# Kernel optimization log

Measured on AMD Instinct MI355X. Metric: run time of the kernel, lower is better.

The kernel has to match this reference:

```python
import jax, jax.numpy as jnp
import numpy as np

N_WIRES = 12
DIM = 2 ** N_WIRES  # 4096 = seq_len * embed_dim

_H = np.array([[1, 1], [1, -1]], dtype=np.complex64) / np.sqrt(2.0)
_CNOT = np.array([[1, 0, 0, 0],
                  [0, 1, 0, 0],
                  [0, 0, 0, 1],
                  [0, 0, 1, 0]], dtype=np.complex64)
_SWAP = np.array([[1, 0, 0, 0],
                  [0, 0, 1, 0],
                  [0, 1, 0, 0],
                  [0, 0, 0, 1]], dtype=np.complex64)

def _cp_mat(theta):
    m = np.eye(4, dtype=np.complex64)
    m[3, 3] = np.exp(1j * theta)
    return m

def _apply_gate(state, U, wires):
    # state: (B,) + (2,)*N_WIRES ; U: (2^k, 2^k) acting on `wires` (wire 0 = MSB = axis 1)
    k = len(wires)
    src = [w + 1 for w in wires]
    dst = list(range(1, k + 1))
    st = jnp.moveaxis(state, src, dst)
    sh = st.shape
    st = st.reshape(sh[0], 2 ** k, -1)
    st = jnp.einsum('ij,bjr->bir', jnp.asarray(U), st)
    return jnp.moveaxis(st.reshape(sh), dst, src)

def _cnot_ring(state):
    for i in range(N_WIRES):
        state = _apply_gate(state, _CNOT, [i, (i + 1) % N_WIRES])
    return state

def _qft(state):
    for m in range(N_WIRES - 1, 0, -1):
        state = _apply_gate(state, _H, [m])
        for i in range(m):
            state = _apply_gate(state, _cp_mat(np.pi / 2 ** (m - i)), [i, m])
    for i in range(N_WIRES // 2):
        state = _apply_gate(state, _SWAP, [i, N_WIRES - i - 1])
    return state

def _full_unitary(state, U):
    # dense 2^n x 2^n unitary over the whole register: psi' = U @ psi
    b = state.shape[0]
    flat = state.reshape(b, DIM)
    return jnp.einsum('ij,bj->bi', U, flat).reshape(state.shape)

def setup_inputs() -> dict:
    key = jax.random.key(0)
    k1, k2, k3 = jax.random.split(key, 3)
    x = jax.random.normal(k1, (128, 64, 64), dtype=jnp.float32)
    scale = DIM ** -0.5  # keep applied matrices roughly norm-preserving
    U_re = jax.random.normal(k2, (4, DIM, DIM), dtype=jnp.float32) * scale
    U_im = jax.random.normal(k3, (4, DIM, DIM), dtype=jnp.float32) * scale
    return {"x": x, "U_re": U_re, "U_im": U_im}

def reference(x, U_re, U_im):
    B, S, E = x.shape
    flat = x.reshape(B, S * E)
    pad = DIM - flat.shape[1]
    if pad > 0:
        flat = jnp.pad(flat, ((0, 0), (0, pad)))
    # StateEncoder: L2-normalize and lift to complex statevector
    norm = jnp.sqrt(jnp.sum(flat * flat, axis=-1, keepdims=True))
    psi = (flat / norm).astype(jnp.complex64)
    state = psi.reshape((B,) + (2,) * N_WIRES)
    U = (U_re + 1j * U_im).astype(jnp.complex64)
    # vqc(0)
    state = _full_unitary(state, U[0])
    state = _cnot_ring(state)
    state = _full_unitary(state, U[1])
    # qft
    state = _qft(state)
    # vqc(1)
    state = _full_unitary(state, U[2])
    state = _cnot_ring(state)
    state = _full_unitary(state, U[3])
    out = jnp.abs(state.reshape(B, DIM))
    return out.reshape(B, S, E)
```

## Files before the change

kernel.cpp:

```cpp
#include <hip/hip_runtime.h>
#include <hip/hip_bf16.h>
#include <math.h>

#define N_WIRES 12
#define DIM     4096
#define BATCH   128
#define BD      (BATCH*DIM)
#define BM      128
#define BN      32
#define BK      64
#define KS      4
#define KCHUNK  (DIM / KS)

typedef __attribute__((ext_vector_type(4))) float f32x4;
typedef __attribute__((ext_vector_type(4))) unsigned int u32x4;
typedef __bf16 bf16x8 __attribute__((ext_vector_type(8)));
typedef __attribute__((ext_vector_type(8))) unsigned short us8;

__device__ __forceinline__ f32x4 mfma16(bf16x8 a, bf16x8 b, f32x4 c){
  return __builtin_amdgcn_mfma_f32_16x16x32_bf16(a, b, c, 0, 0, 0);
}

__device__ __forceinline__ void gload16(const void* g, void* l){
  __builtin_amdgcn_global_load_lds(
    (const __attribute__((address_space(1))) unsigned int*)g,
    (__attribute__((address_space(3))) unsigned int*)l, 16, 0, 0);
}

__device__ __forceinline__ float bf2f(unsigned short u){
  union { unsigned int i; float f; } cv; cv.i = ((unsigned int)u) << 16; return cv.f;
}

__device__ __forceinline__ int swz(int j, int b){
  return (j & ~63) | (((((j >> 3) & 7) ^ (b & 7))) << 3) | (j & 7);
}

__global__ void k_normalize(const float* __restrict__ x, __hip_bfloat16* __restrict__ dst){
  const int b = blockIdx.x, t = threadIdx.x;
  const float4* xr = reinterpret_cast<const float4*>(x + (size_t)b * DIM);
  float4 v[4];
  float ss = 0.f;
  #pragma unroll
  for (int r = 0; r < 4; ++r){
    v[r] = xr[t*4 + r];
    ss += v[r].x*v[r].x + v[r].y*v[r].y + v[r].z*v[r].z + v[r].w*v[r].w;
  }
  #pragma unroll
  for (int off = 32; off > 0; off >>= 1) ss += __shfl_down(ss, off);
  __shared__ float sred[4];
  if ((t & 63) == 0) sred[t >> 6] = ss;
  __syncthreads();
  const float inv = 1.f / sqrtf(sred[0] + sred[1] + sred[2] + sred[3]);
  #pragma unroll
  for (int h = 0; h < 2; ++h){
    union { __bf16 e[8]; us8 s; } pk;
    const float* vv = reinterpret_cast<const float*>(&v[h*2]);
    #pragma unroll
    for (int j = 0; j < 8; ++j) pk.e[j] = (__bf16)(vv[j] * inv);
    const int j0 = t*16 + h*8;
    *reinterpret_cast<us8*>(dst + (size_t)b*DIM + swz(j0, b)) = pk.s;
  }
}

template<bool CIN>
__global__ __launch_bounds__(256, 2) void k_gemm(
    const float* __restrict__ Ure, const float* __restrict__ Uim,
    const __hip_bfloat16* __restrict__ X, __hip_bfloat16* __restrict__ P)
{
  constexpr int NCC = CIN ? 2 : 1;
  constexpr int NT  = KCHUNK / BK;
  __shared__ __bf16 Xs[2][NCC*BM*BK];
  __shared__ __bf16 Us[2][2*BN*BK];
  const int t = threadIdx.x;
  const int lane = t & 63, wid = t >> 6;
  const int n0 = blockIdx.x * BN;
  const int kb = blockIdx.y * KCHUNK;

  const f32x4 z4 = {0.f,0.f,0.f,0.f};
  f32x4 acc[2][2][2];
  #pragma unroll
  for (int mi = 0; mi < 2; ++mi)
    #pragma unroll
    for (int ni = 0; ni < 2; ++ni){ acc[mi][ni][0] = z4; acc[mi][ni][1] = z4; }

  auto stageX = [&](int kk, int bf){
    #pragma unroll
    for (int r = 0; r < NCC*4; ++r){
      const int idx = r*256 + t;
      const int c = idx >> 10, ci = idx & 1023;
      const int row = ci >> 3, sc = ci & 7;
      gload16(X + (size_t)c*BD + (size_t)row*DIM + kb + kk + sc*8, &Xs[bf][idx*8]);
    }
  };
  auto loadU = [&](int kk, float4 (&uv)[4]){
    #pragma unroll
    for (int r = 0; r < 4; ++r){
      const int idx = r*256 + t;
      const int c = idx >> 9, ci = idx & 511;
      const int row = ci >> 4, q = ci & 15;
      const float* us = c ? Uim : Ure;
      uv[r] = *reinterpret_cast<const float4*>(us + (size_t)(n0 + row)*DIM + kb + kk + q*4);
    }
  };
  auto writeU = [&](const float4 (&uv)[4], int bf){
    #pragma unroll
    for (int r = 0; r < 4; ++r){
      const int idx = r*256 + t;
      const int c = idx >> 9, ci = idx & 511;
      const int row = ci >> 4, q = ci & 15;
      union { __bf16 h[4]; unsigned long long u; } pk;
      pk.h[0]=(__bf16)uv[r].x; pk.h[1]=(__bf16)uv[r].y;
      pk.h[2]=(__bf16)uv[r].z; pk.h[3]=(__bf16)uv[r].w;
      const int e = (((q >> 1) ^ (row & 7)) << 3) | ((q & 1) << 2);
      *reinterpret_cast<unsigned long long*>(&Us[bf][c*BN*BK + row*BK + e]) = pk.u;
    }
  };
  auto compute = [&](int bf){
    #pragma unroll
    for (int ks = 0; ks < 2; ++ks){
      const int lc = ks*4 + (lane >> 4);
      bf16x8 ar[2], ai[2], br[2], bi[2];
      #pragma unroll
      for (int mi = 0; mi < 2; ++mi){
        const int row = wid*32 + mi*16 + (lane & 15);
        const int off = row*BK + ((lc ^ (row & 7)) << 3);
        ar[mi] = *reinterpret_cast<const bf16x8*>(&Xs[bf][off]);
        if (CIN) ai[mi] = *reinterpret_cast<const bf16x8*>(&Xs[bf][BM*BK + off]);
      }
      #pragma unroll
      for (int ni = 0; ni < 2; ++ni){
        const int row = ni*16 + (lane & 15);
        const int off = row*BK + ((lc ^ (row & 7)) << 3);
        br[ni] = *reinterpret_cast<const bf16x8*>(&Us[bf][off]);
        bi[ni] = *reinterpret_cast<const bf16x8*>(&Us[bf][BN*BK + off]);
      }
      #pragma unroll
      for (int mi = 0; mi < 2; ++mi){
        bf16x8 an = ar[mi];
        if (CIN){
          const u32x4 negu = __builtin_bit_cast(u32x4, ai[mi]) ^ 0x80008000u;
          an = __builtin_bit_cast(bf16x8, negu);
        }
        #pragma unroll
        for (int ni = 0; ni < 2; ++ni){
          acc[mi][ni][0] = mfma16(ar[mi], br[ni], acc[mi][ni][0]);
          acc[mi][ni][1] = mfma16(ar[mi], bi[ni], acc[mi][ni][1]);
          if (CIN){
            acc[mi][ni][0] = mfma16(an,     bi[ni], acc[mi][ni][0]);
            acc[mi][ni][1] = mfma16(ai[mi], br[ni], acc[mi][ni][1]);
          }
        }
      }
    }
  };

  float4 uvA[4], uvB[4];
  stageX(0, 0);
  loadU(0, uvA);

#define GSTEP(TT, UVC, UVN)                                                    \
  {                                                                            \
    const int cur = (TT) & 1;                                                  \
    if ((TT) + 1 < NT){                                                        \
      stageX(((TT)+1)*BK, cur ^ 1);                                            \
      loadU(((TT)+1)*BK, UVN);                                                 \
      if constexpr (CIN) asm volatile("s_waitcnt vmcnt(12)" ::: "memory");     \
      else               asm volatile("s_waitcnt vmcnt(8)"  ::: "memory");     \
    } else {                                                                   \
      asm volatile("s_waitcnt vmcnt(0)" ::: "memory");                         \
    }                                                                          \
    __builtin_amdgcn_sched_barrier(0);                                         \
    writeU(UVC, cur);                                                          \
    asm volatile("s_waitcnt lgkmcnt(0)" ::: "memory");                         \
    __builtin_amdgcn_s_barrier();                                              \
    compute(cur);                                                              \
    __builtin_amdgcn_sched_barrier(0);                                         \
    __builtin_amdgcn_s_barrier();                                              \
  }

  for (int t2 = 0; t2 < NT; t2 += 2){
    GSTEP(t2,     uvA, uvB);
    GSTEP(t2 + 1, uvB, uvA);
  }
#undef GSTEP

  __hip_bfloat16* pre = P + (size_t)(blockIdx.y*2 + 0)*BD;
  __hip_bfloat16* pim = P + (size_t)(blockIdx.y*2 + 1)*BD;
  #pragma unroll
  for (int mi = 0; mi < 2; ++mi)
    #pragma unroll
    for (int ni = 0; ni < 2; ++ni){
      const int col = n0 + ni*16 + (lane & 15);
      const int m0 = wid*32 + mi*16 + (lane >> 4)*4;
      #pragma unroll
      for (int j = 0; j < 4; ++j){
        pre[(size_t)(m0+j)*DIM + col] = __float2bfloat16(acc[mi][ni][0][j]);
        pim[(size_t)(m0+j)*DIM + col] = __float2bfloat16(acc[mi][ni][1][j]);
      }
    }
}

__device__ __forceinline__ int cnot_dst(int x){
  #pragma unroll
  for (int i = 0; i < 12; ++i){
    const int cb = 11 - i;
    const int tb = 11 - ((i + 1) % 12);
    x ^= ((x >> cb) & 1) << tb;
  }
  return x;
}

__global__ void k_perm(const __hip_bfloat16* __restrict__ P, __hip_bfloat16* __restrict__ dst){
  const int g = blockIdx.x * 256 + threadIdx.x;
  const int b = g >> 9;
  const int m0 = (g & 511) * 8;
  float re[8], im[8];
  #pragma unroll
  for (int j = 0; j < 8; ++j){ re[j] = 0.f; im[j] = 0.f; }
  #pragma unroll
  for (int s = 0; s < KS; ++s){
    const us8 vr = *reinterpret_cast<const us8*>(P + (size_t)(s*2+0)*BD + (size_t)b*DIM + m0);
    const us8 vi = *reinterpret_cast<const us8*>(P + (size_t)(s*2+1)*BD + (size_t)b*DIM + m0);
    #pragma unroll
    for (int j = 0; j < 8; ++j){
      re[j] += bf2f(vr[j]);
      im[j] += bf2f(vi[j]);
    }
  }
  #pragma unroll
  for (int j = 0; j < 8; ++j){
    const int e = swz(cnot_dst(m0 + j), b);
    dst[(size_t)b*DIM + e] = __float2bfloat16(re[j]);
    dst[(size_t)BD + (size_t)b*DIM + e] = __float2bfloat16(im[j]);
  }
}

__global__ void k_abs(const __hip_bfloat16* __restrict__ P, float* __restrict__ dst){
  const int g = blockIdx.x * 256 + threadIdx.x;
  const int b = g >> 9;
  const int m0 = (g & 511) * 8;
  float re[8], im[8];
  #pragma unroll
  for (int j = 0; j < 8; ++j){ re[j] = 0.f; im[j] = 0.f; }
  #pragma unroll
  for (int s = 0; s < KS; ++s){
    const us8 vr = *reinterpret_cast<const us8*>(P + (size_t)(s*2+0)*BD + (size_t)b*DIM + m0);
    const us8 vi = *reinterpret_cast<const us8*>(P + (size_t)(s*2+1)*BD + (size_t)b*DIM + m0);
    #pragma unroll
    for (int j = 0; j < 8; ++j){
      re[j] += bf2f(vr[j]);
      im[j] += bf2f(vi[j]);
    }
  }
  #pragma unroll
  for (int j = 0; j < 8; ++j)
    dst[(size_t)b*DIM + m0 + j] = sqrtf(re[j]*re[j] + im[j]*im[j]);
}

__global__ void k_qft(const __hip_bfloat16* __restrict__ P, __hip_bfloat16* __restrict__ out){
  __shared__ float sre[DIM];
  __shared__ float sim[DIM];
  const int b = blockIdx.x, t = threadIdx.x;
  {
    const int m0 = t * 8;
    float re[8], im[8];
    #pragma unroll
    for (int j = 0; j < 8; ++j){ re[j] = 0.f; im[j] = 0.f; }
    #pragma unroll
    for (int s = 0; s < KS; ++s){
      const us8 vr = *reinterpret_cast<const us8*>(P + (size_t)(s*2+0)*BD + (size_t)b*DIM + m0);
      const us8 vi = *reinterpret_cast<const us8*>(P + (size_t)(s*2+1)*BD + (size_t)b*DIM + m0);
      #pragma unroll
      for (int j = 0; j < 8; ++j){
        re[j] += bf2f(vr[j]);
        im[j] += bf2f(vi[j]);
      }
    }
    #pragma unroll
    for (int j = 0; j < 8; ++j){ sre[m0+j] = re[j]; sim[m0+j] = im[j]; }
  }
  __syncthreads();
  const float rs2 = 0.70710678118654752440f;
  for (int m = 11; m >= 1; --m){
    const int p = 11 - m;
    const int mask = 1 << p;
    for (int q = t; q < 2048; q += 512){
      const int i0 = ((q & ~(mask-1)) << 1) | (q & (mask-1));
      const int i1 = i0 | mask;
      const float r0 = sre[i0], s0 = sim[i0], r1 = sre[i1], s1 = sim[i1];
      sre[i0] = (r0 + r1) * rs2; sim[i0] = (s0 + s1) * rs2;
      sre[i1] = (r0 - r1) * rs2; sim[i1] = (s0 - s1) * rs2;
    }
    __syncthreads();
    for (int q = t; q < 2048; q += 512){
      const int i1 = (((q & ~(mask-1)) << 1) | (q & (mask-1))) | mask;
      int u = i1 >> (p + 1);
      float phi = 0.f, w = 1.57079632679489662f;
      while (u){ if (u & 1) phi += w; w *= 0.5f; u >>= 1; }
      float cc, ss;
      __sincosf(phi, &ss, &cc);
      const float r = sre[i1], q2 = sim[i1];
      sre[i1] = r*cc - q2*ss;
      sim[i1] = r*ss + q2*cc;
    }
    __syncthreads();
  }
  for (int i = t; i < DIM; i += 512){
    const int rsrc = (int)(__brev((unsigned)i) >> 20);
    const int e = swz(i, b);
    out[(size_t)b*DIM + e] = __float2bfloat16(sre[rsrc]);
    out[(size_t)BD + (size_t)b*DIM + e] = __float2bfloat16(sim[rsrc]);
  }
}

extern "C" void kernel_launch(void* const* d_in, const int* in_sizes, int n_in,
                              void* d_out, int out_size, void* d_ws, size_t ws_size,
                              hipStream_t stream){
  const float* x   = (const float*)d_in[0];
  const float* Ure = (const float*)d_in[1];
  const float* Uim = (const float*)d_in[2];
  float* out = (float*)d_out;

  __hip_bfloat16* P  = (__hip_bfloat16*)d_ws;
  __hip_bfloat16* B0 = P + (size_t)KS*2*BD;
  __hip_bfloat16* B1 = B0 + (size_t)2*BD;
  const size_t UST = (size_t)DIM*DIM;
  const dim3 gg(DIM/BN, KS);

  k_normalize<<<BATCH, 256, 0, stream>>>(x, B0);
  k_gemm<false><<<gg, 256, 0, stream>>>(Ure, Uim, B0, P);
  k_perm<<<BD/2048, 256, 0, stream>>>(P, B1);
  k_gemm<true><<<gg, 256, 0, stream>>>(Ure + UST, Uim + UST, B1, P);
  k_qft<<<BATCH, 512, 0, stream>>>(P, B0);
  k_gemm<true><<<gg, 256, 0, stream>>>(Ure + 2*UST, Uim + 2*UST, B0, P);
  k_perm<<<BD/2048, 256, 0, stream>>>(P, B1);
  k_gemm<true><<<gg, 256, 0, stream>>>(Ure + 3*UST, Uim + 3*UST, B1, P);
  k_abs<<<BD/2048, 256, 0, stream>>>(P, out);
}
```

Before: 215.7 us.

## Deepen U prefetch, transpose MFMA output for vector stores, gather-based perm and faster QFT

The GEMM now prefetches the fp32 U tiles two steps ahead with three register buffers and a fully unrolled 16-step schedule with tuned vmcnt waits. It also swaps the MFMA operands so each lane holds consecutive columns, which allows packed 4-wide bf16 stores. k_perm becomes a per-batch LDS kernel that gathers through the inverse CNOT permutation, so its global stores are contiguous 16-byte writes instead of scattered ones. k_qft runs with 1024 threads, computes the phase with a bit reversal instead of a loop, and writes packed vectors. The cost is more register pressure in the GEMM, and the hardcoded wait counts and unroll assume NT=16.

```diff
diff --git a/kernel.cpp b/kernel.cpp
--- a/kernel.cpp
+++ b/kernel.cpp
@@ -16,6 +16,7 @@
 typedef __attribute__((ext_vector_type(4))) unsigned int u32x4;
 typedef __bf16 bf16x8 __attribute__((ext_vector_type(8)));
 typedef __attribute__((ext_vector_type(8))) unsigned short us8;
+typedef __attribute__((ext_vector_type(4))) unsigned short us4;
 
 __device__ __forceinline__ f32x4 mfma16(bf16x8 a, bf16x8 b, f32x4 c){
   return __builtin_amdgcn_mfma_f32_16x16x32_bf16(a, b, c, 0, 0, 0);
@@ -143,45 +144,52 @@
         }
         #pragma unroll
         for (int ni = 0; ni < 2; ++ni){
-          acc[mi][ni][0] = mfma16(ar[mi], br[ni], acc[mi][ni][0]);
-          acc[mi][ni][1] = mfma16(ar[mi], bi[ni], acc[mi][ni][1]);
+          acc[mi][ni][0] = mfma16(br[ni], ar[mi], acc[mi][ni][0]);
+          acc[mi][ni][1] = mfma16(bi[ni], ar[mi], acc[mi][ni][1]);
           if (CIN){
-            acc[mi][ni][0] = mfma16(an,     bi[ni], acc[mi][ni][0]);
-            acc[mi][ni][1] = mfma16(ai[mi], br[ni], acc[mi][ni][1]);
+            acc[mi][ni][0] = mfma16(bi[ni], an,     acc[mi][ni][0]);
+            acc[mi][ni][1] = mfma16(br[ni], ai[mi], acc[mi][ni][1]);
           }
         }
       }
     }
   };
 
-  float4 uvA[4], uvB[4];
+  float4 uvA[4], uvB[4], uvC[4];
+  loadU(0, uvA);
+  loadU(BK, uvB);
   stageX(0, 0);
-  loadU(0, uvA);
-
-#define GSTEP(TT, UVC, UVN)                                                    \
+
+#define GSTEP(TT, UC, UN, WAITS)                                               \
   {                                                                            \
-    const int cur = (TT) & 1;                                                  \
-    if ((TT) + 1 < NT){                                                        \
-      stageX(((TT)+1)*BK, cur ^ 1);                                            \
-      loadU(((TT)+1)*BK, UVN);                                                 \
-      if constexpr (CIN) asm volatile("s_waitcnt vmcnt(12)" ::: "memory");     \
-      else               asm volatile("s_waitcnt vmcnt(8)"  ::: "memory");     \
-    } else {                                                                   \
-      asm volatile("s_waitcnt vmcnt(0)" ::: "memory");                         \
-    }                                                                          \
+    if ((TT) + 1 < NT) stageX(((TT)+1)*BK, ((TT)+1) & 1);                      \
+    if ((TT) + 2 < NT) loadU(((TT)+2)*BK, UN);                                 \
+    asm volatile("s_waitcnt vmcnt(" WAITS ")" ::: "memory");                   \
     __builtin_amdgcn_sched_barrier(0);                                         \
-    writeU(UVC, cur);                                                          \
+    writeU(UC, (TT) & 1);                                                      \
     asm volatile("s_waitcnt lgkmcnt(0)" ::: "memory");                         \
     __builtin_amdgcn_s_barrier();                                              \
-    compute(cur);                                                              \
+    compute((TT) & 1);                                                         \
     __builtin_amdgcn_sched_barrier(0);                                         \
     __builtin_amdgcn_s_barrier();                                              \
   }
 
-  for (int t2 = 0; t2 < NT; t2 += 2){
-    GSTEP(t2,     uvA, uvB);
-    GSTEP(t2 + 1, uvB, uvA);
-  }
+  GSTEP(0,  uvA, uvC, "12")
+  GSTEP(1,  uvB, uvA, "16")
+  GSTEP(2,  uvC, uvB, "16")
+  GSTEP(3,  uvA, uvC, "16")
+  GSTEP(4,  uvB, uvA, "16")
+  GSTEP(5,  uvC, uvB, "16")
+  GSTEP(6,  uvA, uvC, "16")
+  GSTEP(7,  uvB, uvA, "16")
+  GSTEP(8,  uvC, uvB, "16")
+  GSTEP(9,  uvA, uvC, "16")
+  GSTEP(10, uvB, uvA, "16")
+  GSTEP(11, uvC, uvB, "16")
+  GSTEP(12, uvA, uvC, "16")
+  GSTEP(13, uvB, uvA, "16")
+  GSTEP(14, uvC, uvB, "12")
+  GSTEP(15, uvA, uvB, "0")
 #undef GSTEP
 
   __hip_bfloat16* pre = P + (size_t)(blockIdx.y*2 + 0)*BD;
@@ -190,13 +198,16 @@
   for (int mi = 0; mi < 2; ++mi)
     #pragma unroll
     for (int ni = 0; ni < 2; ++ni){
-      const int col = n0 + ni*16 + (lane & 15);
-      const int m0 = wid*32 + mi*16 + (lane >> 4)*4;
+      const int b  = wid*32 + mi*16 + (lane & 15);
+      const int nb = n0 + ni*16 + (lane >> 4)*4;
+      union { __hip_bfloat16 h[4]; us4 v; } pk0, pk1;
       #pragma unroll
       for (int j = 0; j < 4; ++j){
-        pre[(size_t)(m0+j)*DIM + col] = __float2bfloat16(acc[mi][ni][0][j]);
-        pim[(size_t)(m0+j)*DIM + col] = __float2bfloat16(acc[mi][ni][1][j]);
+        pk0.h[j] = __float2bfloat16(acc[mi][ni][0][j]);
+        pk1.h[j] = __float2bfloat16(acc[mi][ni][1][j]);
       }
+      *reinterpret_cast<us4*>(pre + (size_t)b*DIM + nb) = pk0.v;
+      *reinterpret_cast<us4*>(pim + (size_t)b*DIM + nb) = pk1.v;
     }
 }
 
@@ -209,29 +220,50 @@
   }
   return x;
 }
+__device__ __forceinline__ int cnot_inv(int x){
+  #pragma unroll
+  for (int i = 11; i >= 0; --i){
+    const int cb = 11 - i;
+    const int tb = 11 - ((i + 1) % 12);
+    x ^= ((x >> cb) & 1) << tb;
+  }
+  return x;
+}
 
 __global__ void k_perm(const __hip_bfloat16* __restrict__ P, __hip_bfloat16* __restrict__ dst){
-  const int g = blockIdx.x * 256 + threadIdx.x;
-  const int b = g >> 9;
-  const int m0 = (g & 511) * 8;
-  float re[8], im[8];
-  #pragma unroll
-  for (int j = 0; j < 8; ++j){ re[j] = 0.f; im[j] = 0.f; }
-  #pragma unroll
-  for (int s = 0; s < KS; ++s){
-    const us8 vr = *reinterpret_cast<const us8*>(P + (size_t)(s*2+0)*BD + (size_t)b*DIM + m0);
-    const us8 vi = *reinterpret_cast<const us8*>(P + (size_t)(s*2+1)*BD + (size_t)b*DIM + m0);
+  __shared__ float sre[DIM];
+  __shared__ float sim[DIM];
+  const int b = blockIdx.x, t = threadIdx.x;
+  #pragma unroll
+  for (int h = 0; h < 2; ++h){
+    const int m0 = (t*2 + h) * 8;
+    float re[8], im[8];
+    #pragma unroll
+    for (int j = 0; j < 8; ++j){ re[j] = 0.f; im[j] = 0.f; }
+    #pragma unroll
+    for (int s = 0; s < KS; ++s){
+      const us8 vr = *reinterpret_cast<const us8*>(P + (size_t)(s*2+0)*BD + (size_t)b*DIM + m0);
+      const us8 vi = *reinterpret_cast<const us8*>(P + (size_t)(s*2+1)*BD + (size_t)b*DIM + m0);
+      #pragma unroll
+      for (int j = 0; j < 8; ++j){ re[j] += bf2f(vr[j]); im[j] += bf2f(vi[j]); }
+    }
+    #pragma unroll
+    for (int j = 0; j < 8; ++j){ sre[m0+j] = re[j]; sim[m0+j] = im[j]; }
+  }
+  __syncthreads();
+  #pragma unroll
+  for (int h = 0; h < 2; ++h){
+    const int E0 = (t*2 + h) * 8;
+    const int k0 = swz(E0, b);
+    union { __hip_bfloat16 e[8]; us8 s; } pr, pi;
     #pragma unroll
     for (int j = 0; j < 8; ++j){
-      re[j] += bf2f(vr[j]);
-      im[j] += bf2f(vi[j]);
-    }
-  }
-  #pragma unroll
-  for (int j = 0; j < 8; ++j){
-    const int e = swz(cnot_dst(m0 + j), b);
-    dst[(size_t)b*DIM + e] = __float2bfloat16(re[j]);
-    dst[(size_t)BD + (size_t)b*DIM + e] = __float2bfloat16(im[j]);
+      const int m = cnot_inv(k0 + j);
+      pr.e[j] = __float2bfloat16(sre[m]);
+      pi.e[j] = __float2bfloat16(sim[m]);
+    }
+    *reinterpret_cast<us8*>(dst + (size_t)b*DIM + E0) = pr.s;
+    *reinterpret_cast<us8*>(dst + (size_t)BD + (size_t)b*DIM + E0) = pi.s;
   }
 }
 
@@ -247,10 +279,7 @@
     const us8 vr = *reinterpret_cast<const us8*>(P + (size_t)(s*2+0)*BD + (size_t)b*DIM + m0);
     const us8 vi = *reinterpret_cast<const us8*>(P + (size_t)(s*2+1)*BD + (size_t)b*DIM + m0);
     #pragma unroll
-    for (int j = 0; j < 8; ++j){
-      re[j] += bf2f(vr[j]);
-      im[j] += bf2f(vi[j]);
-    }
+    for (int j = 0; j < 8; ++j){ re[j] += bf2f(vr[j]); im[j] += bf2f(vi[j]); }
   }
   #pragma unroll
   for (int j = 0; j < 8; ++j)
@@ -262,29 +291,29 @@
   __shared__ float sim[DIM];
   const int b = blockIdx.x, t = threadIdx.x;
   {
-    const int m0 = t * 8;
-    float re[8], im[8];
-    #pragma unroll
-    for (int j = 0; j < 8; ++j){ re[j] = 0.f; im[j] = 0.f; }
+    const int c  = t >> 9;
+    const int m0 = (t & 511) * 8;
+    float v[8];
+    #pragma unroll
+    for (int j = 0; j < 8; ++j) v[j] = 0.f;
     #pragma unroll
     for (int s = 0; s < KS; ++s){
-      const us8 vr = *reinterpret_cast<const us8*>(P + (size_t)(s*2+0)*BD + (size_t)b*DIM + m0);
-      const us8 vi = *reinterpret_cast<const us8*>(P + (size_t)(s*2+1)*BD + (size_t)b*DIM + m0);
-      #pragma unroll
-      for (int j = 0; j < 8; ++j){
-        re[j] += bf2f(vr[j]);
-        im[j] += bf2f(vi[j]);
-      }
-    }
-    #pragma unroll
-    for (int j = 0; j < 8; ++j){ sre[m0+j] = re[j]; sim[m0+j] = im[j]; }
+      const us8 vv = *reinterpret_cast<const us8*>(P + (size_t)(s*2+c)*BD + (size_t)b*DIM + m0);
+      #pragma unroll
+      for (int j = 0; j < 8; ++j) v[j] += bf2f(vv[j]);
+    }
+    float* s0 = c ? sim : sre;
+    #pragma unroll
+    for (int j = 0; j < 8; ++j) s0[m0+j] = v[j];
   }
   __syncthreads();
   const float rs2 = 0.70710678118654752440f;
+  const float pscale = 3.14159265358979323846f * 0x1p-32f;
   for (int m = 11; m >= 1; --m){
     const int p = 11 - m;
     const int mask = 1 << p;
-    for (int q = t; q < 2048; q += 512){
+    #pragma unroll
+    for (int q = t; q < 2048; q += 1024){
       const int i0 = ((q & ~(mask-1)) << 1) | (q & (mask-1));
       const int i1 = i0 | mask;
       const float r0 = sre[i0], s0 = sim[i0], r1 = sre[i1], s1 = sim[i1];
@@ -292,11 +321,11 @@
       sre[i1] = (r0 - r1) * rs2; sim[i1] = (s0 - s1) * rs2;
     }
     __syncthreads();
-    for (int q = t; q < 2048; q += 512){
+    #pragma unroll
+    for (int q = t; q < 2048; q += 1024){
       const int i1 = (((q & ~(mask-1)) << 1) | (q & (mask-1))) | mask;
-      int u = i1 >> (p + 1);
-      float phi = 0.f, w = 1.57079632679489662f;
-      while (u){ if (u & 1) phi += w; w *= 0.5f; u >>= 1; }
+      const unsigned u = (unsigned)(i1 >> (p + 1));
+      const float phi = (float)__brev(u) * pscale;
       float cc, ss;
       __sincosf(phi, &ss, &cc);
       const float r = sre[i1], q2 = sim[i1];
@@ -305,11 +334,18 @@
     }
     __syncthreads();
   }
-  for (int i = t; i < DIM; i += 512){
-    const int rsrc = (int)(__brev((unsigned)i) >> 20);
-    const int e = swz(i, b);
-    out[(size_t)b*DIM + e] = __float2bfloat16(sre[rsrc]);
-    out[(size_t)BD + (size_t)b*DIM + e] = __float2bfloat16(sim[rsrc]);
+  {
+    const int c  = t >> 9;
+    const int E0 = (t & 511) * 8;
+    const int i0 = swz(E0, b);
+    const float* s0 = c ? sim : sre;
+    union { __hip_bfloat16 e[8]; us8 s; } pk;
+    #pragma unroll
+    for (int j = 0; j < 8; ++j){
+      const int rsrc = (int)(__brev((unsigned)(i0 + j)) >> 20);
+      pk.e[j] = __float2bfloat16(s0[rsrc]);
+    }
+    *reinterpret_cast<us8*>(out + (size_t)c*BD + (size_t)b*DIM + E0) = pk.s;
   }
 }
 
@@ -329,11 +365,11 @@
 
   k_normalize<<<BATCH, 256, 0, stream>>>(x, B0);
   k_gemm<false><<<gg, 256, 0, stream>>>(Ure, Uim, B0, P);
-  k_perm<<<BD/2048, 256, 0, stream>>>(P, B1);
+  k_perm<<<BATCH, 256, 0, stream>>>(P, B1);
   k_gemm<true><<<gg, 256, 0, stream>>>(Ure + UST, Uim + UST, B1, P);
-  k_qft<<<BATCH, 512, 0, stream>>>(P, B0);
+  k_qft<<<BATCH, 1024, 0, stream>>>(P, B0);
   k_gemm<true><<<gg, 256, 0, stream>>>(Ure + 2*UST, Uim + 2*UST, B0, P);
-  k_perm<<<BD/2048, 256, 0, stream>>>(P, B1);
+  k_perm<<<BATCH, 256, 0, stream>>>(P, B1);
   k_gemm<true><<<gg, 256, 0, stream>>>(Ure + 3*UST, Uim + 3*UST, B1, P);
   k_abs<<<BD/2048, 256, 0, stream>>>(P, out);
 }
```

Measured after the change: 192.2 us. 1.12x faster.
